# Kernel tuning notes

Measured on AMD Instinct MI355X. Metric: run time of the kernel, lower is better.

Reference implementation:

```python
import jax, jax.numpy as jnp
import numpy as np

C_IN = 32
C_OUT = 64
B, H, W = 4, 128, 128


def _dwconv(x, w, b, pad):
    # x: [B, C, H, W], w: [C*k_mult, 1, K, K] (torch OIHW, groups=C), b: [C*k_mult]
    y = jax.lax.conv_general_dilated(
        x, w, window_strides=(1, 1), padding=[(pad, pad), (pad, pad)],
        dimension_numbers=("NCHW", "OIHW", "NCHW"),
        feature_group_count=x.shape[1])
    return y + b[None, :, None, None]


def setup_inputs() -> dict:
    key = jax.random.key(0)
    ks = jax.random.split(key, 9)
    x = jax.random.normal(ks[0], (B, C_IN, H, W), dtype=jnp.float32)
    # inner 3x3 depthwise weights: shifted-identity init (each of 9 taps picks one position)
    w3 = np.zeros((C_IN * 9, 1, 3, 3), dtype=np.float32)
    for c in range(C_IN):
        for k in range(9):
            w3[c * 9 + k, 0, k // 3, k % 3] = 1.0
    w3 = jnp.asarray(w3)
    b3 = jax.random.normal(ks[1], (C_IN * 9,), dtype=jnp.float32) * 0.02
    # ring convs: module zero-inits them, but they remain learnable params; use
    # small random values so the conv math (and its gradients) are exercised.
    w5 = jax.random.normal(ks[2], (C_IN * 16, 1, 5, 5), dtype=jnp.float32) * 0.05
    b5 = jax.random.normal(ks[3], (C_IN * 16,), dtype=jnp.float32) * 0.02
    w7 = jax.random.normal(ks[4], (C_IN * 24, 1, 7, 7), dtype=jnp.float32) * 0.05
    b7 = jax.random.normal(ks[5], (C_IN * 24,), dtype=jnp.float32) * 0.02
    # final 1x1 pointwise conv: [C_OUT, C_IN*49]
    wf = jax.random.normal(ks[6], (C_OUT, C_IN * 49), dtype=jnp.float32) * (1.0 / np.sqrt(C_IN * 49))
    bf = jax.random.normal(ks[7], (C_OUT,), dtype=jnp.float32) * 0.02
    return {"x": x, "w3": w3, "b3": b3, "w5": w5, "b5": b5,
            "w7": w7, "b7": b7, "wf": wf, "bf": bf}


def reference(x, w3, b3, w5, b5, w7, b7, wf, bf):
    inner = _dwconv(x, w3, b3, pad=1)   # [B, C*9,  H, W]
    ring5 = _dwconv(x, w5, b5, pad=2)   # [B, C*16, H, W]
    ring7 = _dwconv(x, w7, b7, pad=3)   # [B, C*24, H, W]
    feats = jnp.concatenate([inner, ring5, ring7], axis=1)  # [B, C*49, H, W]
    out = jnp.einsum("bchw,oc->bohw", feats, wf) + bf[None, :, None, None]
    return out
```

## Files before the change

kernel.cpp:

```cpp
#include <hip/hip_runtime.h>

#define BATCH 4
#define HH 128
#define WW 128

typedef __attribute__((ext_vector_type(8))) short bf16x8;
typedef __attribute__((ext_vector_type(4))) float f32x4;

__device__ __forceinline__ unsigned short f2bf(float f) {
    unsigned int u = __float_as_uint(f);
    unsigned int r = (u + 0x7FFFu + ((u >> 16) & 1u)) >> 16;
    return (unsigned short)r;
}

__global__ __launch_bounds__(256) void prep_all(
    const float* __restrict__ w3, const float* __restrict__ b3,
    const float* __restrict__ w5, const float* __restrict__ b5,
    const float* __restrict__ w7, const float* __restrict__ b7,
    const float* __restrict__ wf, const float* __restrict__ bf,
    unsigned short* __restrict__ Weff2, float* __restrict__ Beff)
{
    const int tid = threadIdx.x;
    if (blockIdx.x < 32) {
        const int c = blockIdx.x;
        __shared__ float lwf[64 * 49];
        __shared__ float lw3[9 * 9];
        __shared__ float lw5[16 * 25];
        __shared__ float lw7[24 * 49];

        for (int idx = tid; idx < 64 * 49; idx += 256) {
            int o = idx / 49, k = idx % 49;
            int j = (k < 9)  ? (c * 9 + k)
                  : (k < 25) ? (288 + c * 16 + (k - 9))
                             : (800 + c * 24 + (k - 25));
            lwf[idx] = wf[o * 1568 + j];
        }
        for (int idx = tid; idx < 81;   idx += 256) lw3[idx] = w3[c * 81 + idx];
        for (int idx = tid; idx < 400;  idx += 256) lw5[idx] = w5[c * 400 + idx];
        for (int idx = tid; idx < 1176; idx += 256) lw7[idx] = w7[c * 1176 + idx];
        __syncthreads();

        for (int idx = tid; idx < 49 * 64; idx += 256) {
            int o = idx % 64;
            int p = idx / 64;
            int ky = p / 7, kx = p % 7;
            float acc = 0.f;
            if (ky >= 2 && ky <= 4 && kx >= 2 && kx <= 4) {
                int pos = (ky - 2) * 3 + (kx - 2);
                #pragma unroll
                for (int k = 0; k < 9; ++k)
                    acc += lwf[o * 49 + k] * lw3[k * 9 + pos];
            }
            if (ky >= 1 && ky <= 5 && kx >= 1 && kx <= 5) {
                int pos = (ky - 1) * 5 + (kx - 1);
                #pragma unroll
                for (int k = 0; k < 16; ++k)
                    acc += lwf[o * 49 + 9 + k] * lw5[k * 25 + pos];
            }
            {
                int pos = ky * 7 + kx;
                #pragma unroll
                for (int k = 0; k < 24; ++k)
                    acc += lwf[o * 49 + 25 + k] * lw7[k * 49 + pos];
            }
            Weff2[(p * 64 + o) * 32 + c] = f2bf(acc);
        }
    } else {
        const int o = blockIdx.x - 32;
        float acc = 0.f;
        for (int j = tid; j < 1568; j += 256) {
            float bj = (j < 288) ? b3[j] : (j < 800) ? b5[j - 288] : b7[j - 800];
            acc += wf[o * 1568 + j] * bj;
        }
        __shared__ float red[256];
        red[tid] = acc;
        __syncthreads();
        for (int s = 128; s > 0; s >>= 1) {
            if (tid < s) red[tid] += red[tid + s];
            __syncthreads();
        }
        if (tid == 0) Beff[o] = red[0] + bf[o];
    }
}

#define XROWS 14
#define XCOLS 22
#define PXW 17
#define NPX (XROWS * XCOLS)
#define LDSW (NPX * PXW)

__global__ __launch_bounds__(256, 2) void conv_mfma(
    const float* __restrict__ x, const unsigned short* __restrict__ Weff2,
    const float* __restrict__ Beff, float* __restrict__ out)
{
    __shared__ unsigned int xw[LDSW];
    const int b  = blockIdx.z;
    const int h0 = blockIdx.y * 8;
    const int w0 = blockIdx.x * 16;
    const int tid = threadIdx.x;

    const float* xb = x + (size_t)b * 32 * HH * WW;
    for (int e = tid; e < NPX * 16; e += 256) {
        int cp  = e / NPX;
        int pxl = e - cp * NPX;
        int row = pxl / XCOLS, col = pxl - row * XCOLS;
        int h = h0 + row - 3, w = w0 + col - 3;
        float f0 = 0.f, f1 = 0.f;
        if (h >= 0 && h < HH && w >= 0 && w < WW) {
            f0 = xb[((2 * cp) * HH + h) * WW + w];
            f1 = xb[((2 * cp + 1) * HH + h) * WW + w];
        }
        xw[pxl * PXW + cp] = (unsigned int)f2bf(f0) | ((unsigned int)f2bf(f1) << 16);
    }
    __syncthreads();

    const int lane = tid & 63;
    const int n = lane & 15;
    const int g = lane >> 4;
    const int wid = __builtin_amdgcn_readfirstlane(tid >> 6);
    const int ocbase  = (wid & 1) * 32;
    const int row_grp = (wid >> 1) * 4;

    f32x4 acc[2][4];
    #pragma unroll
    for (int t = 0; t < 2; ++t)
        #pragma unroll
        for (int f = 0; f < 4; ++f)
            acc[t][f] = (f32x4){0.f, 0.f, 0.f, 0.f};

    const char* Wp = (const char*)Weff2;
    const int aoff0 = (ocbase + n) * 64 + g * 16;
    const int aoff1 = aoff0 + 16 * 64;

    for (int ky = 0; ky < 7; ++ky) {
        #pragma unroll
        for (int kx = 0; kx < 7; ++kx) {
            const int p = ky * 7 + kx;
            bf16x8 a0 = *(const bf16x8*)(Wp + p * 4096 + aoff0);
            bf16x8 a1 = *(const bf16x8*)(Wp + p * 4096 + aoff1);
            #pragma unroll
            for (int f = 0; f < 4; ++f) {
                const int lrow = row_grp + f + ky;
                const int widx = (lrow * XCOLS + n + kx) * PXW + g * 4;
                bf16x8 bfrag = *(const bf16x8*)&xw[widx];
                acc[0][f] = __builtin_amdgcn_mfma_f32_16x16x32_bf16(
                    a0, bfrag, acc[0][f], 0, 0, 0);
                acc[1][f] = __builtin_amdgcn_mfma_f32_16x16x32_bf16(
                    a1, bfrag, acc[1][f], 0, 0, 0);
            }
        }
    }

    const int oc_r = ocbase + g * 4;
    const int wcol = w0 + n;
    #pragma unroll
    for (int t = 0; t < 2; ++t) {
        #pragma unroll
        for (int r = 0; r < 4; ++r) {
            const int oc = oc_r + t * 16 + r;
            const float bias = Beff[oc];
            #pragma unroll
            for (int f = 0; f < 4; ++f) {
                const int h = h0 + row_grp + f;
                out[(((size_t)b * 64 + oc) * HH + h) * WW + wcol] =
                    acc[t][f][r] + bias;
            }
        }
    }
}

extern "C" void kernel_launch(void* const* d_in, const int* in_sizes, int n_in,
                              void* d_out, int out_size, void* d_ws, size_t ws_size,
                              hipStream_t stream) {
    const float* x  = (const float*)d_in[0];
    const float* w3 = (const float*)d_in[1];
    const float* b3 = (const float*)d_in[2];
    const float* w5 = (const float*)d_in[3];
    const float* b5 = (const float*)d_in[4];
    const float* w7 = (const float*)d_in[5];
    const float* b7 = (const float*)d_in[6];
    const float* wf = (const float*)d_in[7];
    const float* bf = (const float*)d_in[8];
    float* outp = (float*)d_out;

    unsigned short* Weff2 = (unsigned short*)d_ws;
    float* Beff = (float*)((char*)d_ws + 49 * 64 * 32 * sizeof(unsigned short));

    prep_all<<<96, 256, 0, stream>>>(w3, b3, w5, b5, w7, b7, wf, bf, Weff2, Beff);

    dim3 grid(WW / 16, HH / 8, BATCH);
    conv_mfma<<<grid, 256, 0, stream>>>(x, Weff2, Beff, outp);
}
```

Measured before the change: 113.6 us.

## Pre-convert input to channel-last bf16 and enlarge conv tiles to 16 rows

The prep kernel gains 512 extra blocks that transpose x into a pixel-major bf16 buffer, so the conv kernel can load its halo tile with 16-byte vector loads instead of strided fp32 gathers with per-element conversion. The conv tile grows to 16x16 output pixels with 512 threads, which cuts the halo overhead per block. The padded LDS stride is removed, which may bring back bank conflicts on the B-fragment reads. The extra transposed buffer costs one more global read and write pass over x.

```diff
diff --git a/kernel.cpp b/kernel.cpp
--- a/kernel.cpp
+++ b/kernel.cpp
@@ -13,11 +13,14 @@
     return (unsigned short)r;
 }
 
+
 __global__ __launch_bounds__(256) void prep_all(
+    const float* __restrict__ x,
     const float* __restrict__ w3, const float* __restrict__ b3,
     const float* __restrict__ w5, const float* __restrict__ b5,
     const float* __restrict__ w7, const float* __restrict__ b7,
     const float* __restrict__ wf, const float* __restrict__ bf,
+    unsigned short* __restrict__ xb16,
     unsigned short* __restrict__ Weff2, float* __restrict__ Beff)
 {
     const int tid = threadIdx.x;
@@ -65,7 +68,7 @@
             }
             Weff2[(p * 64 + o) * 32 + c] = f2bf(acc);
         }
-    } else {
+    } else if (blockIdx.x < 96) {
         const int o = blockIdx.x - 32;
         float acc = 0.f;
         for (int j = tid; j < 1568; j += 256) {
@@ -80,37 +83,52 @@
             __syncthreads();
         }
         if (tid == 0) Beff[o] = red[0] + bf[o];
-    }
-}
-
-#define XROWS 14
+    } else {
+        const int row = blockIdx.x - 96;
+        const int b = row >> 7, h = row & 127;
+        __shared__ float ls[32 * 129];
+        const float* xr = x + ((size_t)(b * 32) * HH + h) * WW;
+        for (int idx = tid; idx < 32 * 128; idx += 256) {
+            int c = idx >> 7, w = idx & 127;
+            ls[c * 129 + w] = xr[(size_t)c * HH * WW + w];
+        }
+        __syncthreads();
+        unsigned int* dst = (unsigned int*)xb16 + ((size_t)(b * 128 + h) * 128) * 16;
+        for (int wi = tid; wi < 2048; wi += 256) {
+            int w = wi >> 4, cw = wi & 15;
+            float f0 = ls[(2 * cw) * 129 + w];
+            float f1 = ls[(2 * cw + 1) * 129 + w];
+            dst[wi] = (unsigned int)f2bf(f0) | ((unsigned int)f2bf(f1) << 16);
+        }
+    }
+}
+
+#define XROWS 22
 #define XCOLS 22
-#define PXW 17
 #define NPX (XROWS * XCOLS)
-#define LDSW (NPX * PXW)
-
-__global__ __launch_bounds__(256, 2) void conv_mfma(
-    const float* __restrict__ x, const unsigned short* __restrict__ Weff2,
+typedef __attribute__((ext_vector_type(4))) unsigned int uint4v;
+
+__global__ __launch_bounds__(512, 4) void conv_mfma(
+    const unsigned short* __restrict__ xb16,
+    const unsigned short* __restrict__ Weff2,
     const float* __restrict__ Beff, float* __restrict__ out)
 {
-    __shared__ unsigned int xw[LDSW];
+    __shared__ unsigned int xw[NPX * 16];
     const int b  = blockIdx.z;
-    const int h0 = blockIdx.y * 8;
+    const int h0 = blockIdx.y * 16;
     const int w0 = blockIdx.x * 16;
     const int tid = threadIdx.x;
 
-    const float* xb = x + (size_t)b * 32 * HH * WW;
-    for (int e = tid; e < NPX * 16; e += 256) {
-        int cp  = e / NPX;
-        int pxl = e - cp * NPX;
-        int row = pxl / XCOLS, col = pxl - row * XCOLS;
+    const uint4v* xbv = (const uint4v*)xb16 + (size_t)b * 128 * 128 * 4;
+    const uint4v zero4 = (uint4v){0u, 0u, 0u, 0u};
+    for (int e = tid; e < NPX * 4; e += 512) {
+        int px = e >> 2, cg = e & 3;
+        int row = px / XCOLS, col = px - row * XCOLS;
         int h = h0 + row - 3, w = w0 + col - 3;
-        float f0 = 0.f, f1 = 0.f;
-        if (h >= 0 && h < HH && w >= 0 && w < WW) {
-            f0 = xb[((2 * cp) * HH + h) * WW + w];
-            f1 = xb[((2 * cp + 1) * HH + h) * WW + w];
-        }
-        xw[pxl * PXW + cp] = (unsigned int)f2bf(f0) | ((unsigned int)f2bf(f1) << 16);
+        uint4v v = zero4;
+        if (h >= 0 && h < HH && w >= 0 && w < WW)
+            v = xbv[((h * WW + w) << 2) + cg];
+        *(uint4v*)&xw[px * 16 + cg * 4] = v;
     }
     __syncthreads();
 
@@ -141,7 +159,7 @@
             #pragma unroll
             for (int f = 0; f < 4; ++f) {
                 const int lrow = row_grp + f + ky;
-                const int widx = (lrow * XCOLS + n + kx) * PXW + g * 4;
+                const int widx = (lrow * XCOLS + n + kx) * 16 + g * 4;
                 bf16x8 bfrag = *(const bf16x8*)&xw[widx];
                 acc[0][f] = __builtin_amdgcn_mfma_f32_16x16x32_bf16(
                     a0, bfrag, acc[0][f], 0, 0, 0);
@@ -183,11 +201,13 @@
     const float* bf = (const float*)d_in[8];
     float* outp = (float*)d_out;
 
-    unsigned short* Weff2 = (unsigned short*)d_ws;
-    float* Beff = (float*)((char*)d_ws + 49 * 64 * 32 * sizeof(unsigned short));
-
-    prep_all<<<96, 256, 0, stream>>>(w3, b3, w5, b5, w7, b7, wf, bf, Weff2, Beff);
-
-    dim3 grid(WW / 16, HH / 8, BATCH);
-    conv_mfma<<<grid, 256, 0, stream>>>(x, Weff2, Beff, outp);
-}
+    unsigned short* xb16  = (unsigned short*)d_ws;
+    unsigned short* Weff2 = (unsigned short*)((char*)d_ws + 4194304);
+    float*          Beff  = (float*)((char*)d_ws + 4194304 + 200704);
+
+    prep_all<<<608, 256, 0, stream>>>(x, w3, b3, w5, b5, w7, b7, wf, bf,
+                                      xb16, Weff2, Beff);
+
+    dim3 grid(WW / 16, HH / 16, BATCH);
+    conv_mfma<<<grid, 512, 0, stream>>>(xb16, Weff2, Beff, outp);
+}
```

Result: faster. 107.6 us (-5.3%).
